# Kernel optimization log

Hardware: AMD Instinct MI355X
Metric: run time of the kernel (lower is better)

## Reference

```python
import jax, jax.numpy as jnp
import numpy as np

K = 20          # k_neighbors from __init__
B, N = 4, 8192  # batch, points
EPS_NORM = 1e-12  # F.normalize eps


def setup_inputs() -> dict:
    key = jax.random.key(0)
    ks = jax.random.split(key, 4)
    point_cloud = jax.random.normal(ks[0], (B, N, 3), dtype=jnp.float32)
    vis_mask = jnp.ones((B, N), dtype=bool)

    def init_w(k, shape):
        return jax.random.normal(k, shape, dtype=jnp.float32) / np.sqrt(shape[1]).astype(np.float32)

    W1 = init_w(ks[1], (64, 10));  b1 = jnp.zeros((64,),  jnp.float32)
    W2 = init_w(ks[2], (128, 64)); b2 = jnp.zeros((128,), jnp.float32)
    W3 = init_w(ks[3], (256, 128)); b3 = jnp.zeros((256,), jnp.float32)
    return {"point_cloud": point_cloud, "vis_mask": vis_mask,
            "W1": W1, "b1": b1, "W2": W2, "b2": b2, "W3": W3, "b3": b3}


def _knn(points, k):
    # points: (B,N,3) -> knn_idx (B,N,k), excluding self (smallest distance)
    sq = jnp.sum(points * points, axis=-1)  # (B,N)
    d = sq[:, :, None] + sq[:, None, :] - 2.0 * jnp.einsum('bnd,bmd->bnm', points, points)
    _, idx = jax.lax.top_k(-d, k + 1)       # k+1 smallest distances
    return idx[:, :, 1:k + 1]


def _geometry(points, k):
    # local neighborhood features + PCA normals + curvature
    knn_idx = _knn(points, k)                              # (B,N,k)
    bidx = jnp.arange(points.shape[0])[:, None, None]
    neighbors = points[bidx, knn_idx]                      # (B,N,k,3)
    local = neighbors - points[:, :, None, :]              # (B,N,k,3)
    centered = local - jnp.mean(local, axis=2, keepdims=True)
    cov = jnp.einsum('bnki,bnkj->bnij', centered, centered)  # (B,N,3,3)
    w, v = jnp.linalg.eigh(cov)  # eigenvalues ascending
    # normal = eigenvector of smallest eigenvalue (== last right-singular vector of torch.svd)
    normals = v[..., :, 0]                                 # (B,N,3)
    dot = jnp.sum(normals * (-points), axis=-1, keepdims=True)
    normals = jnp.where(dot < 0, -normals, normals)
    normals = normals / jnp.maximum(jnp.linalg.norm(normals, axis=-1, keepdims=True), EPS_NORM)
    curvature = (w[..., 0] / (jnp.sum(w, axis=-1) + 1e-10))[..., None]  # (B,N,1)
    return local, normals, curvature


def reference(point_cloud, vis_mask, W1, b1, W2, b2, W3, b3):
    # vis_mask is all-True (equal visible count per batch required by source reshape)
    visible = jnp.where(vis_mask[..., None], point_cloud, 0.0)  # (B,N,3)
    local, normals, curvature = _geometry(visible, K)
    combined = jnp.concatenate(
        [visible, normals, curvature, jnp.mean(local, axis=2)], axis=-1)  # (B,N,10)
    # 1x1 Conv1d stack == pointwise MLP
    h = jax.nn.relu(jnp.einsum('bnc,oc->bno', combined, W1) + b1)
    h = jax.nn.relu(jnp.einsum('bnc,oc->bno', h, W2) + b2)
    h = jnp.einsum('bnc,oc->bno', h, W3) + b3
    return jnp.transpose(h, (0, 2, 1))  # (B,256,N)
```

## Files before the change

kernel.cpp:

```cpp
#include <hip/hip_runtime.h>
#include <stdint.h>

#define NPTS 8192
#define NBATCH 4
#define KNN_K 20
typedef unsigned long long ull;
typedef unsigned int uint;
typedef float v2f __attribute__((ext_vector_type(2)));

__device__ __forceinline__ v2f pk_fma(v2f a, v2f b, v2f c) {
  v2f d;
  asm("v_pk_fma_f32 %0, %1, %2, %3" : "=v"(d) : "v"(a), "v"(b), "v"(c));
  return d;
}
__device__ __forceinline__ v2f pk_mul(v2f a, v2f b) {
  v2f d;
  asm("v_pk_mul_f32 %0, %1, %2" : "=v"(d) : "v"(a), "v"(b));
  return d;
}

static constexpr int NBIN = 1024;
__device__ __forceinline__ int binof(float x) {
  int b = (int)floorf((x + 5.5f) * (1024.0f / 11.0f));
  return min(max(b, 0), NBIN - 1);
}

__global__ __launch_bounds__(256)
void zero_hist(uint* __restrict__ hist) {
  int g = blockIdx.x * 256 + threadIdx.x;
  if (g < NBATCH * NBIN) hist[g] = 0;
}

__global__ __launch_bounds__(256)
void prep_kernel(const float* __restrict__ pc, float4* __restrict__ p4,
                 uint* __restrict__ hist,
                 const float* __restrict__ W1, const float* __restrict__ W2,
                 const float* __restrict__ W3, float* __restrict__ T1,
                 float* __restrict__ T2, float* __restrict__ T3) {
  int g = blockIdx.x * 256 + threadIdx.x;
  if (g < NBATCH * NPTS) {
    float x = pc[g * 3 + 0], y = pc[g * 3 + 1], z = pc[g * 3 + 2];
    p4[g] = make_float4(x, y, z, fmaf(z, z, fmaf(y, y, x * x)));
    atomicAdd(&hist[(g >> 13) * NBIN + binof(x)], 1u);
  }
  if (g < 640) {
    T1[(g % 10) * 64 + g / 10] = W1[g];
  } else if (g < 640 + 8192) {
    int q = g - 640;
    T2[(q % 64) * 128 + q / 64] = W2[q];
  } else if (g < 640 + 8192 + 32768) {
    int q = g - 8832;
    T3[(q % 128) * 256 + q / 128] = W3[q];
  }
}

__global__ __launch_bounds__(1024)
void scan_kernel(const uint* __restrict__ hist, uint* __restrict__ offv,
                 uint* __restrict__ cursor) {
  const int b = blockIdx.x;
  const int t = threadIdx.x;
  __shared__ uint buf[2][NBIN];
  uint cnt = hist[b * NBIN + t];
  buf[0][t] = cnt;
  __syncthreads();
  int src = 0;
#pragma unroll
  for (int off = 1; off < NBIN; off <<= 1) {
    uint v = buf[src][t];
    if (t >= off) v += buf[src][t - off];
    buf[src ^ 1][t] = v;
    __syncthreads();
    src ^= 1;
  }
  uint inc = buf[src][t];
  uint exc = inc - cnt;
  offv[b * (NBIN + 1) + t] = exc;
  cursor[b * NBIN + t]     = exc;
  if (t == NBIN - 1) offv[b * (NBIN + 1) + NBIN] = inc;
}

__global__ __launch_bounds__(256)
void scatter_kernel(const float4* __restrict__ p4, uint* __restrict__ cursor,
                    float4* __restrict__ p4s, uint* __restrict__ o32) {
  int g = blockIdx.x * 256 + threadIdx.x;
  if (g >= NBATCH * NPTS) return;
  int b = g >> 13;
  float4 v = p4[g];
  uint pos = atomicAdd(&cursor[b * NBIN + binof(v.x)], 1u);
  p4s[(size_t)b * NPTS + pos] = v;
  o32[(size_t)b * NPTS + pos] = (uint)(g & (NPTS - 1));
}

static constexpr int ST   = 512;
static constexpr int RPW  = 4;
static constexpr int BR   = 16;
static constexpr int QCAP = 128;
static constexpr int TPAD = 66;

__global__ __launch_bounds__(256, 5)
void knn_kernel(const float4* __restrict__ p4s, const uint* __restrict__ o32,
                const uint* __restrict__ offv, int* __restrict__ knn_out) {
  const int tid  = threadIdx.x;
  const int lane = tid & 63;
  const int wv   = tid >> 6;
  const int row0 = blockIdx.x * BR + wv * RPW;
  const int bat  = row0 >> 13;
  const float4* __restrict__ Ps = p4s + (size_t)bat * NPTS;
  const uint*   __restrict__ Os = o32 + (size_t)bat * NPTS;
  const int rbase = row0 & (NPTS - 1);
  const int qrow0 = wv * RPW;

  __shared__ float plx[ST], ply[ST], plz[ST], plw[ST];
  __shared__ uint  qidx[BR][QCAP];
  __shared__ ull   kb2[4][4 * TPAD];
  __shared__ float thrv[4][RPW];
  __shared__ uint  qn[BR];
  __shared__ float wred[2][BR];
  __shared__ int   iwin[2];

  v2f rx2[RPW], ry2[RPW], rz2[RPW];
  float rqx[RPW], rpw[RPW];
#pragma unroll
  for (int r = 0; r < RPW; ++r) {
    float4 v = Ps[rbase + r];
    rx2[r] = (v2f){v.x, v.x};
    ry2[r] = (v2f){v.y, v.y};
    rz2[r] = (v2f){v.z, v.z};
    rqx[r] = v.x; rpw[r] = v.w;
  }
  const v2f m2 = {-2.0f, -2.0f};
  if (tid < BR) qn[tid] = 0;

#define STAGEW(base)                                                       \
  {                                                                        \
    float4 v = Ps[(base) + tid];                                           \
    plx[tid] = v.x; ply[tid] = v.y; plz[tid] = v.z; plw[tid] = v.w;        \
    v = Ps[(base) + tid + 256];                                            \
    plx[tid + 256] = v.x; ply[tid + 256] = v.y;                            \
    plz[tid + 256] = v.z; plw[tid + 256] = v.w;                            \
  }

  const int blk0 = (blockIdx.x * BR) & (NPTS - 1);
  const int c0   = min(max(blk0 + BR / 2 - 1024, 0), NPTS - 2048);

  float dmin[RPW];
#pragma unroll
  for (int r = 0; r < RPW; ++r) dmin[r] = __int_as_float(0x7f800000);

  for (int s = 0; s < 4; ++s) {
    __syncthreads();
    STAGEW(c0 + s * ST)
    __syncthreads();
#pragma unroll
    for (int tl = 0; tl < ST / 128; ++tl) {
      const int o = tl * 128 + 2 * lane;
      v2f x01 = *(const v2f*)&plx[o];
      v2f y01 = *(const v2f*)&ply[o];
      v2f z01 = *(const v2f*)&plz[o];
      v2f w01 = *(const v2f*)&plw[o];
#pragma unroll
      for (int r = 0; r < RPW; ++r) {
        v2f dot = pk_fma(rz2[r], z01, pk_fma(ry2[r], y01, pk_mul(rx2[r], x01)));
        v2f dp  = pk_fma(m2, dot, w01);
        dmin[r] = fminf(dmin[r], fminf(dp.x, dp.y));
      }
    }
  }

#pragma unroll
  for (int r = 0; r < RPW; ++r) {
    uint u  = __float_as_uint(dmin[r]);
    uint mk = u ^ (uint)(((int)u >> 31) | 0x80000000);
    kb2[wv][r * TPAD + lane] = ((ull)mk << 6) | (uint)lane;
  }
  __syncthreads();
  {
    const int rr = lane >> 4, jj = lane & 15;
    const ull* kp = &kb2[wv][rr * TPAD];
    ull e0 = kp[jj], e1 = kp[jj + 16], e2 = kp[jj + 32], e3 = kp[jj + 48];
    uint r0 = 0, r1 = 0, r2 = 0, r3 = 0;
    for (int i = 0; i < 64; ++i) {
      ull vi = kp[i];
      r0 += (uint)(vi < e0); r1 += (uint)(vi < e1);
      r2 += (uint)(vi < e2); r3 += (uint)(vi < e3);
    }
#define UNMAP(k) __uint_as_float(((uint)((k) >> 6)) ^ ((~((uint)((int)((uint)((k) >> 6)) >> 31))) | 0x80000000u))
    if (r0 == 20) thrv[wv][rr] = UNMAP(e0);
    if (r1 == 20) thrv[wv][rr] = UNMAP(e1);
    if (r2 == 20) thrv[wv][rr] = UNMAP(e2);
    if (r3 == 20) thrv[wv][rr] = UNMAP(e3);
#undef UNMAP
  }
  __syncthreads();
  float thr[RPW];
#pragma unroll
  for (int r = 0; r < RPW; ++r) thr[r] = thrv[wv][r] + 3e-5f;

  if (lane < RPW) {
    const int r = lane;
    float r2v = fmaxf(thr[r] + rpw[r], 0.0f);
    float rad = sqrtf(fmaf(r2v, 1.0001f, 1e-5f));
    wred[0][wv * RPW + r] = rqx[r] - rad - 1e-6f;
    wred[1][wv * RPW + r] = rqx[r] + rad + 1e-6f;
  }
  __syncthreads();
  if (tid == 0) {
    float lo = wred[0][0], hi = wred[1][0];
    for (int i = 1; i < BR; ++i) {
      lo = fminf(lo, wred[0][i]);
      hi = fmaxf(hi, wred[1][i]);
    }
    iwin[0] = (int)offv[bat * (NBIN + 1) + binof(lo)];
    iwin[1] = (int)offv[bat * (NBIN + 1) + binof(hi) + 1];
  }
  __syncthreads();
  const int wlo = iwin[0], whi = iwin[1];
  const int nst = (whi - wlo + ST - 1) / ST;

  for (int s = 0; s < nst; ++s) {
    __syncthreads();
    {
      int i0 = wlo + s * ST + tid;
      if (i0 < whi) {
        float4 v = Ps[i0];
        plx[tid] = v.x; ply[tid] = v.y; plz[tid] = v.z; plw[tid] = v.w;
      } else {
        plx[tid] = 0.0f; ply[tid] = 0.0f; plz[tid] = 0.0f;
        plw[tid] = __int_as_float(0x7f800000);
      }
      i0 += 256;
      if (i0 < whi) {
        float4 v = Ps[i0];
        plx[tid + 256] = v.x; ply[tid + 256] = v.y;
        plz[tid + 256] = v.z; plw[tid + 256] = v.w;
      } else {
        plx[tid + 256] = 0.0f; ply[tid + 256] = 0.0f; plz[tid + 256] = 0.0f;
        plw[tid + 256] = __int_as_float(0x7f800000);
      }
    }
    __syncthreads();
#pragma unroll
    for (int tl = 0; tl < ST / 128; ++tl) {
      const int o  = tl * 128 + 2 * lane;
      const int cb = wlo + s * ST + o;
      v2f x01 = *(const v2f*)&plx[o];
      v2f y01 = *(const v2f*)&ply[o];
      v2f z01 = *(const v2f*)&plz[o];
      v2f w01 = *(const v2f*)&plw[o];
#pragma unroll
      for (int r = 0; r < RPW; ++r) {
        v2f dot = pk_fma(rz2[r], z01, pk_fma(ry2[r], y01, pk_mul(rx2[r], x01)));
        v2f dp  = pk_fma(m2, dot, w01);
        if (dp.x <= thr[r]) {
          uint slot = atomicAdd(&qn[qrow0 + r], 1u);
          if (slot < QCAP) qidx[qrow0 + r][slot] = (uint)cb;
        }
        if (dp.y <= thr[r]) {
          uint slot = atomicAdd(&qn[qrow0 + r], 1u);
          if (slot < QCAP) qidx[qrow0 + r][slot] = (uint)(cb + 1);
        }
      }
    }
  }
  __syncthreads();

  for (int r = 0; r < RPW; ++r) {
    const float4 me = Ps[rbase + r];
    const uint orow = Os[rbase + r];
    const int cnt   = (int)(qn[qrow0 + r] < (uint)QCAP ? qn[qrow0 + r] : (uint)QCAP);

    ull k0 = ~0ull, k1 = ~0ull;
    uint i0 = 0, i1 = 0;
    if (lane < cnt) {
      uint si = qidx[qrow0 + r][lane];
      float4 Q  = Ps[si];
      i0 = Os[si];
      float dot = fmaf(me.z, Q.z, fmaf(me.y, Q.y, me.x * Q.x));
      float d   = fmaxf(fmaf(-2.0f, dot, me.w + Q.w), 0.0f);
      k0 = ((ull)__float_as_uint(d) << 32) | i0;
    }
    if (lane + 64 < cnt) {
      uint si = qidx[qrow0 + r][lane + 64];
      float4 Q  = Ps[si];
      i1 = Os[si];
      float dot = fmaf(me.z, Q.z, fmaf(me.y, Q.y, me.x * Q.x));
      float d   = fmaxf(fmaf(-2.0f, dot, me.w + Q.w), 0.0f);
      k1 = ((ull)__float_as_uint(d) << 32) | i1;
    }
    kb2[wv][lane]      = k0;
    kb2[wv][lane + 64] = k1;
    __syncthreads();

    uint r0 = 0, r1 = 0;
    for (int j = 0; j < cnt; ++j) {
      ull kj = kb2[wv][j];
      r0 += (uint)(kj < k0);
      r1 += (uint)(kj < k1);
    }
    const size_t obase = ((size_t)bat * NPTS + orow) * KNN_K;
    if (lane < cnt && r0 >= 1 && r0 <= 20) knn_out[obase + (r0 - 1)] = (int)i0;
    if (lane + 64 < cnt && r1 >= 1 && r1 <= 20) knn_out[obase + (r1 - 1)] = (int)i1;
    __syncthreads();
  }
#undef STAGEW
}

__global__ __launch_bounds__(256, 2)
void geom_mlp_kernel(const float4* __restrict__ p4,
                     const int* __restrict__ knn,
                     const float* __restrict__ wt1, const float* __restrict__ b1,
                     const float* __restrict__ wt2, const float* __restrict__ b2,
                     const float* __restrict__ wt3, const float* __restrict__ b3,
                     float* __restrict__ out) {
  __shared__ float comb[64][11];
  __shared__ float h1s[64][65];
  __shared__ float h2s[64][131];

  const int tid = threadIdx.x;
  const int p0  = blockIdx.x * 64;

  if (tid < 64) {
    const int gid = p0 + tid;
    const int b = gid >> 13, n = gid & (NPTS - 1);
    const float4* __restrict__ P = p4 + (size_t)b * NPTS;
    const float4 me = P[n];
    const float px = me.x, py = me.y, pz = me.z;

    double sx = 0, sy = 0, sz = 0;
    double sxx = 0, sxy = 0, sxz = 0, syy = 0, syz = 0, szz = 0;
    const int* __restrict__ nb = knn + (size_t)gid * KNN_K;
#pragma unroll 4
    for (int k = 0; k < KNN_K; ++k) {
      float4 q = P[nb[k]];
      double qx = (double)q.x, qy = (double)q.y, qz = (double)q.z;
      sx += qx; sy += qy; sz += qz;
      sxx += qx * qx; sxy += qx * qy; sxz += qx * qz;
      syy += qy * qy; syz += qy * qz; szz += qz * qz;
    }
    const double mx = sx / KNN_K, my = sy / KNN_K, mz = sz / KNN_K;
    const double a00 = sxx - KNN_K * mx * mx;
    const double a01 = sxy - KNN_K * mx * my;
    const double a02 = sxz - KNN_K * mx * mz;
    const double a11 = syy - KNN_K * my * my;
    const double a12 = syz - KNN_K * my * mz;
    const double a22 = szz - KNN_K * mz * mz;

    const double qd = (a00 + a11 + a22) / 3.0;
    const double p1 = a01 * a01 + a02 * a02 + a12 * a12;
    const double d00 = a00 - qd, d11 = a11 - qd, d22 = a22 - qd;
    const double p2 = d00 * d00 + d11 * d11 + d22 * d22 + 2.0 * p1;

    double l0 = qd, l1 = qd, l2 = qd;
    double vx = 1.0, vy = 0.0, vz = 0.0;
    if (p2 > 0.0) {
      const double p  = sqrt(p2 / 6.0);
      const double ip = 1.0 / p;
      const double b00 = d00 * ip, b01 = a01 * ip, b02 = a02 * ip;
      const double b11 = d11 * ip, b12 = a12 * ip, b22 = d22 * ip;
      double detB = b00 * (b11 * b22 - b12 * b12)
                  - b01 * (b01 * b22 - b12 * b02)
                  + b02 * (b01 * b12 - b11 * b02);
      double r = 0.5 * detB;
      r = fmin(1.0, fmax(-1.0, r));
      const double phi = acos(r) / 3.0;
      l2 = qd + 2.0 * p * cos(phi);
      l0 = qd + 2.0 * p * cos(phi + 2.0943951023931953);
      l1 = 3.0 * qd - l0 - l2;

      const double m00 = a00 - l0, m11 = a11 - l0, m22 = a22 - l0;
      const double r0x = m00, r0y = a01, r0z = a02;
      const double r1x = a01, r1y = m11, r1z = a12;
      const double r2x = a02, r2y = a12, r2z = m22;
      double c0x = r0y * r1z - r0z * r1y, c0y = r0z * r1x - r0x * r1z, c0z = r0x * r1y - r0y * r1x;
      double c1x = r0y * r2z - r0z * r2y, c1y = r0z * r2x - r0x * r2z, c1z = r0x * r2y - r0y * r2x;
      double c2x = r1y * r2z - r1z * r2y, c2y = r1z * r2x - r1x * r2z, c2z = r1x * r2y - r1y * r2x;
      double n0 = c0x * c0x + c0y * c0y + c0z * c0z;
      double n1 = c1x * c1x + c1y * c1y + c1z * c1z;
      double n2 = c2x * c2x + c2y * c2y + c2z * c2z;
      double bx = c0x, by = c0y, bz = c0z, bn = n0;
      if (n1 > bn) { bx = c1x; by = c1y; bz = c1z; bn = n1; }
      if (n2 > bn) { bx = c2x; by = c2y; bz = c2z; bn = n2; }
      if (bn > 1e-300) {
        const double innv = 1.0 / sqrt(bn);
        vx = bx * innv; vy = by * innv; vz = bz * innv;
      }
    }
    const double dp = vx * (double)px + vy * (double)py + vz * (double)pz;
    if (dp > 0.0) { vx = -vx; vy = -vy; vz = -vz; }

    const double curv = l0 / (l0 + l1 + l2 + 1e-10);

    comb[tid][0] = px; comb[tid][1] = py; comb[tid][2] = pz;
    comb[tid][3] = (float)vx; comb[tid][4] = (float)vy; comb[tid][5] = (float)vz;
    comb[tid][6] = (float)curv;
    comb[tid][7] = (float)(mx - (double)px);
    comb[tid][8] = (float)(my - (double)py);
    comb[tid][9] = (float)(mz - (double)pz);
  }
  __syncthreads();

  const int pt = tid & 63;
  const int wq = tid >> 6;

  {
    const int ob = __builtin_amdgcn_readfirstlane(wq * 16);
    v2f acc[8];
#pragma unroll
    for (int h = 0; h < 8; ++h) acc[h] = *(const v2f*)&b1[ob + 2 * h];
    for (int k = 0; k < 10; ++k) {
      float x = comb[pt][k];
      v2f x2 = {x, x};
      const float* wrow = &wt1[k * 64 + ob];
#pragma unroll
      for (int h = 0; h < 8; ++h)
        acc[h] = pk_fma(*(const v2f*)&wrow[2 * h], x2, acc[h]);
    }
#pragma unroll
    for (int h = 0; h < 8; ++h) {
      h1s[pt][ob + 2 * h]     = fmaxf(acc[h].x, 0.0f);
      h1s[pt][ob + 2 * h + 1] = fmaxf(acc[h].y, 0.0f);
    }
  }
  __syncthreads();

  {
    const int ob = __builtin_amdgcn_readfirstlane(wq * 32);
    v2f acc[16];
#pragma unroll
    for (int h = 0; h < 16; ++h) acc[h] = *(const v2f*)&b2[ob + 2 * h];
    for (int k = 0; k < 64; ++k) {
      float x = h1s[pt][k];
      v2f x2 = {x, x};
      const float* wrow = &wt2[k * 128 + ob];
#pragma unroll
      for (int h = 0; h < 16; ++h)
        acc[h] = pk_fma(*(const v2f*)&wrow[2 * h], x2, acc[h]);
    }
#pragma unroll
    for (int h = 0; h < 16; ++h) {
      h2s[pt][ob + 2 * h]     = fmaxf(acc[h].x, 0.0f);
      h2s[pt][ob + 2 * h + 1] = fmaxf(acc[h].y, 0.0f);
    }
  }
  __syncthreads();

  {
    const int ob = __builtin_amdgcn_readfirstlane(wq * 64);
    v2f acc[32];
#pragma unroll
    for (int h = 0; h < 32; ++h) acc[h] = *(const v2f*)&b3[ob + 2 * h];
    for (int k = 0; k < 128; ++k) {
      float x = h2s[pt][k];
      v2f x2 = {x, x};
      const float* wrow = &wt3[k * 256 + ob];
#pragma unroll
      for (int h = 0; h < 32; ++h)
        acc[h] = pk_fma(*(const v2f*)&wrow[2 * h], x2, acc[h]);
    }
    const int gpt = p0 + pt;
    const int b = gpt >> 13, n = gpt & (NPTS - 1);
#pragma unroll
    for (int h = 0; h < 32; ++h) {
      out[((size_t)(b * 256 + ob + 2 * h)) * NPTS + n]     = acc[h].x;
      out[((size_t)(b * 256 + ob + 2 * h + 1)) * NPTS + n] = acc[h].y;
    }
  }
}

extern "C" void kernel_launch(void* const* d_in, const int* in_sizes, int n_in,
                              void* d_out, int out_size, void* d_ws, size_t ws_size,
                              hipStream_t stream) {
  const float* pc = (const float*)d_in[0];
  const float* W1 = (const float*)d_in[2];
  const float* b1 = (const float*)d_in[3];
  const float* W2 = (const float*)d_in[4];
  const float* b2 = (const float*)d_in[5];
  const float* W3 = (const float*)d_in[6];
  const float* b3 = (const float*)d_in[7];

  char* ws = (char*)d_ws;
  int*    knn  = (int*)(ws + 0);
  float4* p4   = (float4*)(ws + 2621440);
  float4* p4s  = (float4*)(ws + 3145728);
  uint*   o32  = (uint*)(ws + 3670016);
  uint*   hist = (uint*)(ws + 3801088);
  uint*   offv = (uint*)(ws + 3817472);
  uint*   curs = (uint*)(ws + 3833872);
  float*  wt1  = (float*)(ws + 3850256);
  float*  wt2  = (float*)(ws + 3852816);
  float*  wt3  = (float*)(ws + 3885584);
  float*  outp = (float*)d_out;

  zero_hist<<<dim3(16), dim3(256), 0, stream>>>(hist);
  prep_kernel<<<dim3(163), dim3(256), 0, stream>>>(pc, p4, hist, W1, W2, W3,
                                                   wt1, wt2, wt3);
  scan_kernel<<<dim3(NBATCH), dim3(1024), 0, stream>>>(hist, offv, curs);
  scatter_kernel<<<dim3(128), dim3(256), 0, stream>>>(p4, curs, p4s, o32);
  knn_kernel<<<dim3(NBATCH * NPTS / BR), dim3(256), 0, stream>>>(p4s, o32, offv, knn);
  geom_mlp_kernel<<<dim3(NBATCH * NPTS / 64), dim3(256), 0, stream>>>(
      p4, knn, wt1, b1, wt2, b2, wt3, b3, outp);
}
```

Measured before the change: 191.5 us.

## Split geometry stage into its own fully occupied kernel before the MLP

The fused geometry+MLP kernel ran the double-precision PCA on only 64 of 256 threads per block, leaving three waves idle during that phase. The geometry step now runs as a separate kernel with one point per thread and writes the 10-feature vectors to a global workspace buffer. The MLP kernel then loads those features into shared memory and raises its occupancy hint from 2 to 3 blocks per CU. This adds a kernel launch and a global round trip of about 1.3 MB of intermediate features.

```diff
diff --git a/kernel.cpp b/kernel.cpp
--- a/kernel.cpp
+++ b/kernel.cpp
@@ -305,98 +305,105 @@
 #undef STAGEW
 }
 
-__global__ __launch_bounds__(256, 2)
-void geom_mlp_kernel(const float4* __restrict__ p4,
-                     const int* __restrict__ knn,
-                     const float* __restrict__ wt1, const float* __restrict__ b1,
-                     const float* __restrict__ wt2, const float* __restrict__ b2,
-                     const float* __restrict__ wt3, const float* __restrict__ b3,
-                     float* __restrict__ out) {
-  __shared__ float comb[64][11];
+__global__ __launch_bounds__(256)
+void geom_kernel(const float4* __restrict__ p4, const int* __restrict__ knn,
+                 float* __restrict__ comb) {
+  const int gid = blockIdx.x * 256 + threadIdx.x;
+  if (gid >= NBATCH * NPTS) return;
+  const int b = gid >> 13, n = gid & (NPTS - 1);
+  const float4* __restrict__ P = p4 + (size_t)b * NPTS;
+  const float4 me = P[n];
+  const float px = me.x, py = me.y, pz = me.z;
+
+  double sx = 0, sy = 0, sz = 0;
+  double sxx = 0, sxy = 0, sxz = 0, syy = 0, syz = 0, szz = 0;
+  const int* __restrict__ nb = knn + (size_t)gid * KNN_K;
+#pragma unroll 4
+  for (int k = 0; k < KNN_K; ++k) {
+    float4 q = P[nb[k]];
+    double qx = (double)q.x, qy = (double)q.y, qz = (double)q.z;
+    sx += qx; sy += qy; sz += qz;
+    sxx += qx * qx; sxy += qx * qy; sxz += qx * qz;
+    syy += qy * qy; syz += qy * qz; szz += qz * qz;
+  }
+  const double mx = sx / KNN_K, my = sy / KNN_K, mz = sz / KNN_K;
+  const double a00 = sxx - KNN_K * mx * mx;
+  const double a01 = sxy - KNN_K * mx * my;
+  const double a02 = sxz - KNN_K * mx * mz;
+  const double a11 = syy - KNN_K * my * my;
+  const double a12 = syz - KNN_K * my * mz;
+  const double a22 = szz - KNN_K * mz * mz;
+
+  const double qd = (a00 + a11 + a22) / 3.0;
+  const double p1 = a01 * a01 + a02 * a02 + a12 * a12;
+  const double d00 = a00 - qd, d11 = a11 - qd, d22 = a22 - qd;
+  const double p2 = d00 * d00 + d11 * d11 + d22 * d22 + 2.0 * p1;
+
+  double l0 = qd, l1 = qd, l2 = qd;
+  double vx = 1.0, vy = 0.0, vz = 0.0;
+  if (p2 > 0.0) {
+    const double p  = sqrt(p2 / 6.0);
+    const double ip = 1.0 / p;
+    const double b00 = d00 * ip, b01 = a01 * ip, b02 = a02 * ip;
+    const double b11 = d11 * ip, b12 = a12 * ip, b22 = d22 * ip;
+    double detB = b00 * (b11 * b22 - b12 * b12)
+                - b01 * (b01 * b22 - b12 * b02)
+                + b02 * (b01 * b12 - b11 * b02);
+    double r = 0.5 * detB;
+    r = fmin(1.0, fmax(-1.0, r));
+    const double phi = acos(r) / 3.0;
+    l2 = qd + 2.0 * p * cos(phi);
+    l0 = qd + 2.0 * p * cos(phi + 2.0943951023931953);
+    l1 = 3.0 * qd - l0 - l2;
+
+    const double m00 = a00 - l0, m11 = a11 - l0, m22 = a22 - l0;
+    const double r0x = m00, r0y = a01, r0z = a02;
+    const double r1x = a01, r1y = m11, r1z = a12;
+    const double r2x = a02, r2y = a12, r2z = m22;
+    double c0x = r0y * r1z - r0z * r1y, c0y = r0z * r1x - r0x * r1z, c0z = r0x * r1y - r0y * r1x;
+    double c1x = r0y * r2z - r0z * r2y, c1y = r0z * r2x - r0x * r2z, c1z = r0x * r2y - r0y * r2x;
+    double c2x = r1y * r2z - r1z * r2y, c2y = r1z * r2x - r1x * r2z, c2z = r1x * r2y - r1y * r2x;
+    double n0 = c0x * c0x + c0y * c0y + c0z * c0z;
+    double n1 = c1x * c1x + c1y * c1y + c1z * c1z;
+    double n2 = c2x * c2x + c2y * c2y + c2z * c2z;
+    double bx = c0x, by = c0y, bz = c0z, bn = n0;
+    if (n1 > bn) { bx = c1x; by = c1y; bz = c1z; bn = n1; }
+    if (n2 > bn) { bx = c2x; by = c2y; bz = c2z; bn = n2; }
+    if (bn > 1e-300) {
+      const double innv = 1.0 / sqrt(bn);
+      vx = bx * innv; vy = by * innv; vz = bz * innv;
+    }
+  }
+  const double dp = vx * (double)px + vy * (double)py + vz * (double)pz;
+  if (dp > 0.0) { vx = -vx; vy = -vy; vz = -vz; }
+
+  const double curv = l0 / (l0 + l1 + l2 + 1e-10);
+
+  float o[10];
+  o[0] = px; o[1] = py; o[2] = pz;
+  o[3] = (float)vx; o[4] = (float)vy; o[5] = (float)vz;
+  o[6] = (float)curv;
+  o[7] = (float)(mx - (double)px);
+  o[8] = (float)(my - (double)py);
+  o[9] = (float)(mz - (double)pz);
+#pragma unroll
+  for (int i = 0; i < 10; ++i) comb[(size_t)gid * 10 + i] = o[i];
+}
+
+__global__ __launch_bounds__(256, 3)
+void mlp_kernel(const float* __restrict__ comb,
+                const float* __restrict__ wt1, const float* __restrict__ b1,
+                const float* __restrict__ wt2, const float* __restrict__ b2,
+                const float* __restrict__ wt3, const float* __restrict__ b3,
+                float* __restrict__ out) {
+  __shared__ float cmb[64][11];
   __shared__ float h1s[64][65];
   __shared__ float h2s[64][131];
 
   const int tid = threadIdx.x;
   const int p0  = blockIdx.x * 64;
 
-  if (tid < 64) {
-    const int gid = p0 + tid;
-    const int b = gid >> 13, n = gid & (NPTS - 1);
-    const float4* __restrict__ P = p4 + (size_t)b * NPTS;
-    const float4 me = P[n];
-    const float px = me.x, py = me.y, pz = me.z;
-
-    double sx = 0, sy = 0, sz = 0;
-    double sxx = 0, sxy = 0, sxz = 0, syy = 0, syz = 0, szz = 0;
-    const int* __restrict__ nb = knn + (size_t)gid * KNN_K;
-#pragma unroll 4
-    for (int k = 0; k < KNN_K; ++k) {
-      float4 q = P[nb[k]];
-      double qx = (double)q.x, qy = (double)q.y, qz = (double)q.z;
-      sx += qx; sy += qy; sz += qz;
-      sxx += qx * qx; sxy += qx * qy; sxz += qx * qz;
-      syy += qy * qy; syz += qy * qz; szz += qz * qz;
-    }
-    const double mx = sx / KNN_K, my = sy / KNN_K, mz = sz / KNN_K;
-    const double a00 = sxx - KNN_K * mx * mx;
-    const double a01 = sxy - KNN_K * mx * my;
-    const double a02 = sxz - KNN_K * mx * mz;
-    const double a11 = syy - KNN_K * my * my;
-    const double a12 = syz - KNN_K * my * mz;
-    const double a22 = szz - KNN_K * mz * mz;
-
-    const double qd = (a00 + a11 + a22) / 3.0;
-    const double p1 = a01 * a01 + a02 * a02 + a12 * a12;
-    const double d00 = a00 - qd, d11 = a11 - qd, d22 = a22 - qd;
-    const double p2 = d00 * d00 + d11 * d11 + d22 * d22 + 2.0 * p1;
-
-    double l0 = qd, l1 = qd, l2 = qd;
-    double vx = 1.0, vy = 0.0, vz = 0.0;
-    if (p2 > 0.0) {
-      const double p  = sqrt(p2 / 6.0);
-      const double ip = 1.0 / p;
-      const double b00 = d00 * ip, b01 = a01 * ip, b02 = a02 * ip;
-      const double b11 = d11 * ip, b12 = a12 * ip, b22 = d22 * ip;
-      double detB = b00 * (b11 * b22 - b12 * b12)
-                  - b01 * (b01 * b22 - b12 * b02)
-                  + b02 * (b01 * b12 - b11 * b02);
-      double r = 0.5 * detB;
-      r = fmin(1.0, fmax(-1.0, r));
-      const double phi = acos(r) / 3.0;
-      l2 = qd + 2.0 * p * cos(phi);
-      l0 = qd + 2.0 * p * cos(phi + 2.0943951023931953);
-      l1 = 3.0 * qd - l0 - l2;
-
-      const double m00 = a00 - l0, m11 = a11 - l0, m22 = a22 - l0;
-      const double r0x = m00, r0y = a01, r0z = a02;
-      const double r1x = a01, r1y = m11, r1z = a12;
-      const double r2x = a02, r2y = a12, r2z = m22;
-      double c0x = r0y * r1z - r0z * r1y, c0y = r0z * r1x - r0x * r1z, c0z = r0x * r1y - r0y * r1x;
-      double c1x = r0y * r2z - r0z * r2y, c1y = r0z * r2x - r0x * r2z, c1z = r0x * r2y - r0y * r2x;
-      double c2x = r1y * r2z - r1z * r2y, c2y = r1z * r2x - r1x * r2z, c2z = r1x * r2y - r1y * r2x;
-      double n0 = c0x * c0x + c0y * c0y + c0z * c0z;
-      double n1 = c1x * c1x + c1y * c1y + c1z * c1z;
-      double n2 = c2x * c2x + c2y * c2y + c2z * c2z;
-      double bx = c0x, by = c0y, bz = c0z, bn = n0;
-      if (n1 > bn) { bx = c1x; by = c1y; bz = c1z; bn = n1; }
-      if (n2 > bn) { bx = c2x; by = c2y; bz = c2z; bn = n2; }
-      if (bn > 1e-300) {
-        const double innv = 1.0 / sqrt(bn);
-        vx = bx * innv; vy = by * innv; vz = bz * innv;
-      }
-    }
-    const double dp = vx * (double)px + vy * (double)py + vz * (double)pz;
-    if (dp > 0.0) { vx = -vx; vy = -vy; vz = -vz; }
-
-    const double curv = l0 / (l0 + l1 + l2 + 1e-10);
-
-    comb[tid][0] = px; comb[tid][1] = py; comb[tid][2] = pz;
-    comb[tid][3] = (float)vx; comb[tid][4] = (float)vy; comb[tid][5] = (float)vz;
-    comb[tid][6] = (float)curv;
-    comb[tid][7] = (float)(mx - (double)px);
-    comb[tid][8] = (float)(my - (double)py);
-    comb[tid][9] = (float)(mz - (double)pz);
-  }
+  for (int i = tid; i < 640; i += 256) cmb[i / 10][i % 10] = comb[(size_t)p0 * 10 + i];
   __syncthreads();
 
   const int pt = tid & 63;
@@ -408,7 +415,7 @@
 #pragma unroll
     for (int h = 0; h < 8; ++h) acc[h] = *(const v2f*)&b1[ob + 2 * h];
     for (int k = 0; k < 10; ++k) {
-      float x = comb[pt][k];
+      float x = cmb[pt][k];
       v2f x2 = {x, x};
       const float* wrow = &wt1[k * 64 + ob];
 #pragma unroll
@@ -489,6 +496,7 @@
   float*  wt1  = (float*)(ws + 3850256);
   float*  wt2  = (float*)(ws + 3852816);
   float*  wt3  = (float*)(ws + 3885584);
+  float*  comb = (float*)(ws + 4016656);
   float*  outp = (float*)d_out;
 
   zero_hist<<<dim3(16), dim3(256), 0, stream>>>(hist);
@@ -497,6 +505,7 @@
   scan_kernel<<<dim3(NBATCH), dim3(1024), 0, stream>>>(hist, offv, curs);
   scatter_kernel<<<dim3(128), dim3(256), 0, stream>>>(p4, curs, p4s, o32);
   knn_kernel<<<dim3(NBATCH * NPTS / BR), dim3(256), 0, stream>>>(p4s, o32, offv, knn);
-  geom_mlp_kernel<<<dim3(NBATCH * NPTS / 64), dim3(256), 0, stream>>>(
-      p4, knn, wt1, b1, wt2, b2, wt3, b3, outp);
-}
+  geom_kernel<<<dim3(NBATCH * NPTS / 256), dim3(256), 0, stream>>>(p4, knn, comb);
+  mlp_kernel<<<dim3(NBATCH * NPTS / 64), dim3(256), 0, stream>>>(
+      comb, wt1, b1, wt2, b2, wt3, b3, outp);
+}
```

Result: slower. 195.7 us (+2.2%).
